# Kernel tuning notes

Measured on AMD Instinct MI355X. Metric: run time of the kernel, lower is better.

## Reference

```python
import jax, jax.numpy as jnp
import numpy as np

EPS = 1e-8  # matches torch F.cosine_similarity eps


def setup_inputs() -> dict:
    key = jax.random.key(0)
    k1, k2, k3 = jax.random.split(key, 3)
    S, B, H = 16, 512, 2048
    OGLogits = jax.random.normal(k1, (B, H), dtype=jnp.float32)
    enhancedSamplesLogits = jax.random.normal(k2, (S, B, H), dtype=jnp.float32)
    W = jax.random.normal(k3, (H, H), dtype=jnp.float32) * (1.0 / np.sqrt(H))
    b = jnp.zeros((H,), dtype=jnp.float32)
    return {"OGLogits": OGLogits, "enhancedSamplesLogits": enhancedSamplesLogits, "W": W, "b": b}


def reference(OGLogits, enhancedSamplesLogits, W, b):
    # Original torch code builds the full (S*B, B) cosine-similarity matrix and
    # keeps only the diagonal via an eye mask; mathematically that equals the
    # per-pair cosine similarity cos(enhanced[s,b], OG[b]), computed directly here.
    e_norm = jnp.linalg.norm(enhancedSamplesLogits, axis=-1)          # (S, B)
    o_norm = jnp.linalg.norm(OGLogits, axis=-1)                       # (B,)
    dots = jnp.einsum('sbh,bh->sb', enhancedSamplesLogits, OGLogits)  # (S, B)
    sims = dots / jnp.maximum(e_norm * o_norm[None, :], EPS)          # (S, B)
    weighted = enhancedSamplesLogits * sims[..., None]                # (S, B, H)
    weightedRep = weighted.mean(axis=0)                               # (B, H)
    return weightedRep @ W.T + b                                      # (B, H)
```

## Files before the change

kernel.cpp:

```cpp
#include <hip/hip_runtime.h>

#define S_DIM 16
#define B_DIM 512
#define H_DIM 2048
#define EPS 1e-8f

typedef short bf16x8 __attribute__((ext_vector_type(8)));
typedef float f32x4 __attribute__((ext_vector_type(4)));

__device__ __forceinline__ unsigned short f2bf(float f) {
    union { float f; unsigned int u; } v; v.f = f;
    unsigned int u = v.u;
    unsigned int r = (u + 0x7fffu + ((u >> 16) & 1u)) >> 16;
    return (unsigned short)r;
}

__device__ __forceinline__ float dot4(const float4& a, const float4& b) {
    return a.x*b.x + a.y*b.y + a.z*b.z + a.w*b.w;
}

__global__ __launch_bounds__(256) void convert_w_kernel(
    const float* __restrict__ W, unsigned short* __restrict__ Wb) {
    int i = blockIdx.x * 256 + threadIdx.x;
    float4 v = ((const float4*)W)[i];
    ushort4 o;
    o.x = f2bf(v.x); o.y = f2bf(v.y); o.z = f2bf(v.z); o.w = f2bf(v.w);
    ((ushort4*)Wb)[i] = o;
}

__global__ __launch_bounds__(512) void simwrep_kernel(
    const float* __restrict__ OG, const float* __restrict__ E,
    unsigned short* __restrict__ wrep) {
    const int b = blockIdx.x;
    const int t = threadIdx.x;
    const int lane = t & 63;
    const int wave = t >> 6;

    __shared__ float4 buf[8][512];

    const float4* og4 = (const float4*)(OG + (size_t)b * H_DIM);
    float4 og[8];
    float og2 = 0.f;
    #pragma unroll
    for (int i = 0; i < 8; ++i) {
        og[i] = og4[i * 64 + lane];
        og2 += dot4(og[i], og[i]);
    }
    #pragma unroll
    for (int m = 32; m >= 1; m >>= 1) og2 += __shfl_xor(og2, m, 64);
    const float onorm = sqrtf(og2);

    const int s0 = wave * 2, s1 = wave * 2 + 1;
    const float4* e40 = (const float4*)(E + ((size_t)s0 * B_DIM + b) * H_DIM);
    const float4* e41 = (const float4*)(E + ((size_t)s1 * B_DIM + b) * H_DIM);
    float4 e0[8], e1[8];
    float d0 = 0.f, d1 = 0.f, n0 = 0.f, n1 = 0.f;
    #pragma unroll
    for (int i = 0; i < 8; ++i) {
        e0[i] = e40[i * 64 + lane];
        e1[i] = e41[i * 64 + lane];
        d0 += dot4(e0[i], og[i]);
        n0 += dot4(e0[i], e0[i]);
        d1 += dot4(e1[i], og[i]);
        n1 += dot4(e1[i], e1[i]);
    }
    #pragma unroll
    for (int m = 32; m >= 1; m >>= 1) {
        d0 += __shfl_xor(d0, m, 64);
        n0 += __shfl_xor(n0, m, 64);
        d1 += __shfl_xor(d1, m, 64);
        n1 += __shfl_xor(n1, m, 64);
    }
    const float sim0 = d0 / fmaxf(sqrtf(n0) * onorm, EPS);
    const float sim1 = d1 / fmaxf(sqrtf(n1) * onorm, EPS);

    #pragma unroll
    for (int i = 0; i < 8; ++i) {
        float4 p;
        p.x = e0[i].x * sim0 + e1[i].x * sim1;
        p.y = e0[i].y * sim0 + e1[i].y * sim1;
        p.z = e0[i].z * sim0 + e1[i].z * sim1;
        p.w = e0[i].w * sim0 + e1[i].w * sim1;
        buf[wave][i * 64 + lane] = p;
    }
    __syncthreads();

    float4 s = buf[0][t];
    #pragma unroll
    for (int w = 1; w < 8; ++w) {
        float4 v = buf[w][t];
        s.x += v.x; s.y += v.y; s.z += v.z; s.w += v.w;
    }
    const float sc = 1.f / (float)S_DIM;
    ushort4 o;
    o.x = f2bf(s.x * sc); o.y = f2bf(s.y * sc);
    o.z = f2bf(s.z * sc); o.w = f2bf(s.w * sc);
    ((ushort4*)wrep)[(size_t)b * (H_DIM / 4) + t] = o;
}

__global__ __launch_bounds__(256) void gemm_kernel(
    const unsigned short* __restrict__ A, const unsigned short* __restrict__ Bw,
    const float* __restrict__ bias, float* __restrict__ out) {
    const int n0 = blockIdx.x * 64;
    const int m0 = blockIdx.y * 64;

    __shared__ unsigned short As[64][40];
    __shared__ unsigned short Bs[64][40];

    const int t = threadIdx.x;
    const int lane = t & 63;
    const int wave = t >> 6;
    const int wm = (wave & 1) * 32;
    const int wn = (wave >> 1) * 32;
    const int lr = t >> 2;
    const int lq = t & 3;

    const size_t aoff = (size_t)(m0 + lr) * H_DIM + lq * 8;
    const size_t boff = (size_t)(n0 + lr) * H_DIM + lq * 8;

    f32x4 acc00 = {0.f, 0.f, 0.f, 0.f};
    f32x4 acc01 = {0.f, 0.f, 0.f, 0.f};
    f32x4 acc10 = {0.f, 0.f, 0.f, 0.f};
    f32x4 acc11 = {0.f, 0.f, 0.f, 0.f};

    const int row = lane & 15;
    const int q = lane >> 4;

    uint4 av = *(const uint4*)(A + aoff);
    uint4 bv = *(const uint4*)(Bw + boff);

    for (int k0 = 0; k0 < H_DIM; k0 += 32) {
        *(uint4*)&As[lr][lq * 8] = av;
        *(uint4*)&Bs[lr][lq * 8] = bv;
        __syncthreads();
        if (k0 + 32 < H_DIM) {
            av = *(const uint4*)(A + aoff + k0 + 32);
            bv = *(const uint4*)(Bw + boff + k0 + 32);
        }
        bf16x8 a0 = *(const bf16x8*)&As[wm + row][q * 8];
        bf16x8 a1 = *(const bf16x8*)&As[wm + 16 + row][q * 8];
        bf16x8 b0 = *(const bf16x8*)&Bs[wn + row][q * 8];
        bf16x8 b1 = *(const bf16x8*)&Bs[wn + 16 + row][q * 8];
        acc00 = __builtin_amdgcn_mfma_f32_16x16x32_bf16(a0, b0, acc00, 0, 0, 0);
        acc01 = __builtin_amdgcn_mfma_f32_16x16x32_bf16(a0, b1, acc01, 0, 0, 0);
        acc10 = __builtin_amdgcn_mfma_f32_16x16x32_bf16(a1, b0, acc10, 0, 0, 0);
        acc11 = __builtin_amdgcn_mfma_f32_16x16x32_bf16(a1, b1, acc11, 0, 0, 0);
        __syncthreads();
    }

    const int col = lane & 15;
    const float bias0 = bias[n0 + wn + col];
    const float bias1 = bias[n0 + wn + 16 + col];
    #pragma unroll
    for (int r = 0; r < 4; ++r) {
        const int mr = q * 4 + r;
        float* o0 = out + (size_t)(m0 + wm + mr) * H_DIM + n0 + wn;
        float* o1 = out + (size_t)(m0 + wm + 16 + mr) * H_DIM + n0 + wn;
        o0[col]      = acc00[r] + bias0;
        o0[16 + col] = acc01[r] + bias1;
        o1[col]      = acc10[r] + bias0;
        o1[16 + col] = acc11[r] + bias1;
    }
}

extern "C" void kernel_launch(void* const* d_in, const int* in_sizes, int n_in,
                              void* d_out, int out_size, void* d_ws, size_t ws_size,
                              hipStream_t stream) {
    const float* OG   = (const float*)d_in[0];
    const float* E    = (const float*)d_in[1];
    const float* W    = (const float*)d_in[2];
    const float* bias = (const float*)d_in[3];
    float* out = (float*)d_out;

    unsigned short* wrep = (unsigned short*)d_ws;
    unsigned short* Wb   = wrep + (size_t)B_DIM * H_DIM;

    convert_w_kernel<<<(H_DIM * H_DIM / 4) / 256, 256, 0, stream>>>(W, Wb);
    simwrep_kernel<<<B_DIM, 512, 0, stream>>>(OG, E, wrep);
    gemm_kernel<<<dim3(H_DIM / 64, B_DIM / 64), 256, 0, stream>>>(wrep, Wb, bias, out);
}
```

Before: 131.9 us.

## Fuse W bf16 conversion into split-K GEMM and widen simwrep blocks

Removes the separate W fp32-to-bf16 conversion kernel and converts W tiles on the fly while they are loaded into the GEMM. The GEMM is split along K into two halves to double the block count, with a new reduce kernel that sums the partials and adds the bias. The similarity kernel now uses 1024 threads with one wave per sample instead of two samples per wave. In exchange, each W element is read as fp32 by multiple M-blocks and converted repeatedly, and the split-K path adds a fp32 partial buffer write and read.

```diff
diff --git a/kernel.cpp b/kernel.cpp
--- a/kernel.cpp
+++ b/kernel.cpp
@@ -19,16 +19,7 @@
     return a.x*b.x + a.y*b.y + a.z*b.z + a.w*b.w;
 }
 
-__global__ __launch_bounds__(256) void convert_w_kernel(
-    const float* __restrict__ W, unsigned short* __restrict__ Wb) {
-    int i = blockIdx.x * 256 + threadIdx.x;
-    float4 v = ((const float4*)W)[i];
-    ushort4 o;
-    o.x = f2bf(v.x); o.y = f2bf(v.y); o.z = f2bf(v.z); o.w = f2bf(v.w);
-    ((ushort4*)Wb)[i] = o;
-}
-
-__global__ __launch_bounds__(512) void simwrep_kernel(
+__global__ __launch_bounds__(1024) void simwrep_kernel(
     const float* __restrict__ OG, const float* __restrict__ E,
     unsigned short* __restrict__ wrep) {
     const int b = blockIdx.x;
@@ -36,7 +27,7 @@
     const int lane = t & 63;
     const int wave = t >> 6;
 
-    __shared__ float4 buf[8][512];
+    __shared__ float4 buf[16][512];
 
     const float4* og4 = (const float4*)(OG + (size_t)b * H_DIM);
     float4 og[8];
@@ -50,62 +41,56 @@
     for (int m = 32; m >= 1; m >>= 1) og2 += __shfl_xor(og2, m, 64);
     const float onorm = sqrtf(og2);
 
-    const int s0 = wave * 2, s1 = wave * 2 + 1;
-    const float4* e40 = (const float4*)(E + ((size_t)s0 * B_DIM + b) * H_DIM);
-    const float4* e41 = (const float4*)(E + ((size_t)s1 * B_DIM + b) * H_DIM);
-    float4 e0[8], e1[8];
-    float d0 = 0.f, d1 = 0.f, n0 = 0.f, n1 = 0.f;
+    const float4* e4 = (const float4*)(E + ((size_t)wave * B_DIM + b) * H_DIM);
+    float4 e[8];
+    float d = 0.f, n = 0.f;
     #pragma unroll
     for (int i = 0; i < 8; ++i) {
-        e0[i] = e40[i * 64 + lane];
-        e1[i] = e41[i * 64 + lane];
-        d0 += dot4(e0[i], og[i]);
-        n0 += dot4(e0[i], e0[i]);
-        d1 += dot4(e1[i], og[i]);
-        n1 += dot4(e1[i], e1[i]);
+        e[i] = e4[i * 64 + lane];
+        d += dot4(e[i], og[i]);
+        n += dot4(e[i], e[i]);
     }
     #pragma unroll
     for (int m = 32; m >= 1; m >>= 1) {
-        d0 += __shfl_xor(d0, m, 64);
-        n0 += __shfl_xor(n0, m, 64);
-        d1 += __shfl_xor(d1, m, 64);
-        n1 += __shfl_xor(n1, m, 64);
+        d += __shfl_xor(d, m, 64);
+        n += __shfl_xor(n, m, 64);
     }
-    const float sim0 = d0 / fmaxf(sqrtf(n0) * onorm, EPS);
-    const float sim1 = d1 / fmaxf(sqrtf(n1) * onorm, EPS);
+    const float sim = d / fmaxf(sqrtf(n) * onorm, EPS);
 
     #pragma unroll
     for (int i = 0; i < 8; ++i) {
         float4 p;
-        p.x = e0[i].x * sim0 + e1[i].x * sim1;
-        p.y = e0[i].y * sim0 + e1[i].y * sim1;
-        p.z = e0[i].z * sim0 + e1[i].z * sim1;
-        p.w = e0[i].w * sim0 + e1[i].w * sim1;
+        p.x = e[i].x * sim; p.y = e[i].y * sim;
+        p.z = e[i].z * sim; p.w = e[i].w * sim;
         buf[wave][i * 64 + lane] = p;
     }
     __syncthreads();
 
-    float4 s = buf[0][t];
-    #pragma unroll
-    for (int w = 1; w < 8; ++w) {
-        float4 v = buf[w][t];
-        s.x += v.x; s.y += v.y; s.z += v.z; s.w += v.w;
+    if (t < 512) {
+        float4 s = buf[0][t];
+        #pragma unroll
+        for (int w = 1; w < 16; ++w) {
+            float4 v = buf[w][t];
+            s.x += v.x; s.y += v.y; s.z += v.z; s.w += v.w;
+        }
+        const float sc = 1.f / (float)S_DIM;
+        ushort4 o;
+        o.x = f2bf(s.x * sc); o.y = f2bf(s.y * sc);
+        o.z = f2bf(s.z * sc); o.w = f2bf(s.w * sc);
+        ((ushort4*)wrep)[(size_t)b * (H_DIM / 4) + t] = o;
     }
-    const float sc = 1.f / (float)S_DIM;
-    ushort4 o;
-    o.x = f2bf(s.x * sc); o.y = f2bf(s.y * sc);
-    o.z = f2bf(s.z * sc); o.w = f2bf(s.w * sc);
-    ((ushort4*)wrep)[(size_t)b * (H_DIM / 4) + t] = o;
 }
 
-__global__ __launch_bounds__(256) void gemm_kernel(
-    const unsigned short* __restrict__ A, const unsigned short* __restrict__ Bw,
-    const float* __restrict__ bias, float* __restrict__ out) {
+__global__ __launch_bounds__(256) void gemm_splitk_kernel(
+    const unsigned short* __restrict__ A, const float* __restrict__ W,
+    float* __restrict__ partial) {
     const int n0 = blockIdx.x * 64;
     const int m0 = blockIdx.y * 64;
+    const int kz = blockIdx.z;
+    const int kbase = kz * (H_DIM / 2);
 
     __shared__ unsigned short As[64][40];
-    __shared__ unsigned short Bs[64][40];
+    __shared__ unsigned short Ws[64][40];
 
     const int t = threadIdx.x;
     const int lane = t & 63;
@@ -115,8 +100,8 @@
     const int lr = t >> 2;
     const int lq = t & 3;
 
-    const size_t aoff = (size_t)(m0 + lr) * H_DIM + lq * 8;
-    const size_t boff = (size_t)(n0 + lr) * H_DIM + lq * 8;
+    const size_t aoff = (size_t)(m0 + lr) * H_DIM + kbase + lq * 8;
+    const float* wp = W + (size_t)(n0 + lr) * H_DIM + kbase + lq * 8;
 
     f32x4 acc00 = {0.f, 0.f, 0.f, 0.f};
     f32x4 acc01 = {0.f, 0.f, 0.f, 0.f};
@@ -127,20 +112,26 @@
     const int q = lane >> 4;
 
     uint4 av = *(const uint4*)(A + aoff);
-    uint4 bv = *(const uint4*)(Bw + boff);
+    float4 wv0 = *(const float4*)(wp);
+    float4 wv1 = *(const float4*)(wp + 4);
 
-    for (int k0 = 0; k0 < H_DIM; k0 += 32) {
+    for (int k0 = 0; k0 < H_DIM / 2; k0 += 32) {
         *(uint4*)&As[lr][lq * 8] = av;
-        *(uint4*)&Bs[lr][lq * 8] = bv;
+        ushort4 wlo, whi;
+        wlo.x = f2bf(wv0.x); wlo.y = f2bf(wv0.y); wlo.z = f2bf(wv0.z); wlo.w = f2bf(wv0.w);
+        whi.x = f2bf(wv1.x); whi.y = f2bf(wv1.y); whi.z = f2bf(wv1.z); whi.w = f2bf(wv1.w);
+        *(ushort4*)&Ws[lr][lq * 8] = wlo;
+        *(ushort4*)&Ws[lr][lq * 8 + 4] = whi;
         __syncthreads();
-        if (k0 + 32 < H_DIM) {
+        if (k0 + 32 < H_DIM / 2) {
             av = *(const uint4*)(A + aoff + k0 + 32);
-            bv = *(const uint4*)(Bw + boff + k0 + 32);
+            wv0 = *(const float4*)(wp + k0 + 32);
+            wv1 = *(const float4*)(wp + k0 + 36);
         }
         bf16x8 a0 = *(const bf16x8*)&As[wm + row][q * 8];
         bf16x8 a1 = *(const bf16x8*)&As[wm + 16 + row][q * 8];
-        bf16x8 b0 = *(const bf16x8*)&Bs[wn + row][q * 8];
-        bf16x8 b1 = *(const bf16x8*)&Bs[wn + 16 + row][q * 8];
+        bf16x8 b0 = *(const bf16x8*)&Ws[wn + row][q * 8];
+        bf16x8 b1 = *(const bf16x8*)&Ws[wn + 16 + row][q * 8];
         acc00 = __builtin_amdgcn_mfma_f32_16x16x32_bf16(a0, b0, acc00, 0, 0, 0);
         acc01 = __builtin_amdgcn_mfma_f32_16x16x32_bf16(a0, b1, acc01, 0, 0, 0);
         acc10 = __builtin_amdgcn_mfma_f32_16x16x32_bf16(a1, b0, acc10, 0, 0, 0);
@@ -148,19 +139,31 @@
         __syncthreads();
     }
 
+    float* pz = partial + (size_t)kz * B_DIM * H_DIM;
     const int col = lane & 15;
-    const float bias0 = bias[n0 + wn + col];
-    const float bias1 = bias[n0 + wn + 16 + col];
     #pragma unroll
     for (int r = 0; r < 4; ++r) {
         const int mr = q * 4 + r;
-        float* o0 = out + (size_t)(m0 + wm + mr) * H_DIM + n0 + wn;
-        float* o1 = out + (size_t)(m0 + wm + 16 + mr) * H_DIM + n0 + wn;
-        o0[col]      = acc00[r] + bias0;
-        o0[16 + col] = acc01[r] + bias1;
-        o1[col]      = acc10[r] + bias0;
-        o1[16 + col] = acc11[r] + bias1;
+        float* o0 = pz + (size_t)(m0 + wm + mr) * H_DIM + n0 + wn;
+        float* o1 = pz + (size_t)(m0 + wm + 16 + mr) * H_DIM + n0 + wn;
+        o0[col]      = acc00[r];
+        o0[16 + col] = acc01[r];
+        o1[col]      = acc10[r];
+        o1[16 + col] = acc11[r];
     }
+}
+
+__global__ __launch_bounds__(256) void reduce_kernel(
+    const float* __restrict__ partial, const float* __restrict__ bias,
+    float* __restrict__ out) {
+    const int i = blockIdx.x * 256 + threadIdx.x;
+    const float4 a = ((const float4*)partial)[i];
+    const float4 c = ((const float4*)partial)[i + B_DIM * H_DIM / 4];
+    const float4 bs = ((const float4*)bias)[i & (H_DIM / 4 - 1)];
+    float4 o;
+    o.x = a.x + c.x + bs.x; o.y = a.y + c.y + bs.y;
+    o.z = a.z + c.z + bs.z; o.w = a.w + c.w + bs.w;
+    ((float4*)out)[i] = o;
 }
 
 extern "C" void kernel_launch(void* const* d_in, const int* in_sizes, int n_in,
@@ -173,9 +176,9 @@
     float* out = (float*)d_out;
 
     unsigned short* wrep = (unsigned short*)d_ws;
-    unsigned short* Wb   = wrep + (size_t)B_DIM * H_DIM;
+    float* partial = (float*)((char*)d_ws + (size_t)B_DIM * H_DIM * 2);
 
-    convert_w_kernel<<<(H_DIM * H_DIM / 4) / 256, 256, 0, stream>>>(W, Wb);
-    simwrep_kernel<<<B_DIM, 512, 0, stream>>>(OG, E, wrep);
-    gemm_kernel<<<dim3(H_DIM / 64, B_DIM / 64), 256, 0, stream>>>(wrep, Wb, bias, out);
+    simwrep_kernel<<<B_DIM, 1024, 0, stream>>>(OG, E, wrep);
+    gemm_splitk_kernel<<<dim3(H_DIM / 64, B_DIM / 64, 2), 256, 0, stream>>>(wrep, W, partial);
+    reduce_kernel<<<(B_DIM * H_DIM / 4) / 256, 256, 0, stream>>>(partial, bias, out);
 }
```

New measurement: 138.7 us. +5.2%, slower.

## Fuse W bf16 conversion into GEMM tile load and cut simwrep register pressure

Applied to the files above, without the earlier changes.

Removes the separate W-to-bf16 conversion kernel and instead loads fp32 W tiles directly in the GEMM, converting to bf16 in registers before the shared-memory store. This saves a 16MB read and 8MB write plus one launch. The cost is that each W element is now reread in fp32 by all 8 M-blocks (twice the bytes per reread) and converted redundantly. The K tile grows to 64 with padded shared arrays. The simwrep kernel keeps OG in shared memory and processes samples sequentially, which lowers register use and raises occupancy through launch_bounds(512,4).

```diff
diff --git a/kernel.cpp b/kernel.cpp
--- a/kernel.cpp
+++ b/kernel.cpp
@@ -19,16 +19,7 @@
     return a.x*b.x + a.y*b.y + a.z*b.z + a.w*b.w;
 }
 
-__global__ __launch_bounds__(256) void convert_w_kernel(
-    const float* __restrict__ W, unsigned short* __restrict__ Wb) {
-    int i = blockIdx.x * 256 + threadIdx.x;
-    float4 v = ((const float4*)W)[i];
-    ushort4 o;
-    o.x = f2bf(v.x); o.y = f2bf(v.y); o.z = f2bf(v.z); o.w = f2bf(v.w);
-    ((ushort4*)Wb)[i] = o;
-}
-
-__global__ __launch_bounds__(512) void simwrep_kernel(
+__global__ __launch_bounds__(512, 4) void simwrep_kernel(
     const float* __restrict__ OG, const float* __restrict__ E,
     unsigned short* __restrict__ wrep) {
     const int b = blockIdx.x;
@@ -36,53 +27,55 @@
     const int lane = t & 63;
     const int wave = t >> 6;
 
+    __shared__ float4 ogs[512];
     __shared__ float4 buf[8][512];
+    __shared__ float red[8];
 
     const float4* og4 = (const float4*)(OG + (size_t)b * H_DIM);
-    float4 og[8];
+    float4 o = og4[t];
+    ogs[t] = o;
+    float p = dot4(o, o);
+    #pragma unroll
+    for (int m = 32; m >= 1; m >>= 1) p += __shfl_xor(p, m, 64);
+    if (lane == 0) red[wave] = p;
+    __syncthreads();
     float og2 = 0.f;
     #pragma unroll
-    for (int i = 0; i < 8; ++i) {
-        og[i] = og4[i * 64 + lane];
-        og2 += dot4(og[i], og[i]);
-    }
-    #pragma unroll
-    for (int m = 32; m >= 1; m >>= 1) og2 += __shfl_xor(og2, m, 64);
+    for (int w = 0; w < 8; ++w) og2 += red[w];
     const float onorm = sqrtf(og2);
 
-    const int s0 = wave * 2, s1 = wave * 2 + 1;
-    const float4* e40 = (const float4*)(E + ((size_t)s0 * B_DIM + b) * H_DIM);
-    const float4* e41 = (const float4*)(E + ((size_t)s1 * B_DIM + b) * H_DIM);
-    float4 e0[8], e1[8];
-    float d0 = 0.f, d1 = 0.f, n0 = 0.f, n1 = 0.f;
+    float4 acc[8];
     #pragma unroll
-    for (int i = 0; i < 8; ++i) {
-        e0[i] = e40[i * 64 + lane];
-        e1[i] = e41[i * 64 + lane];
-        d0 += dot4(e0[i], og[i]);
-        n0 += dot4(e0[i], e0[i]);
-        d1 += dot4(e1[i], og[i]);
-        n1 += dot4(e1[i], e1[i]);
-    }
-    #pragma unroll
-    for (int m = 32; m >= 1; m >>= 1) {
-        d0 += __shfl_xor(d0, m, 64);
-        n0 += __shfl_xor(n0, m, 64);
-        d1 += __shfl_xor(d1, m, 64);
-        n1 += __shfl_xor(n1, m, 64);
-    }
-    const float sim0 = d0 / fmaxf(sqrtf(n0) * onorm, EPS);
-    const float sim1 = d1 / fmaxf(sqrtf(n1) * onorm, EPS);
+    for (int i = 0; i < 8; ++i) acc[i] = make_float4(0.f, 0.f, 0.f, 0.f);
 
     #pragma unroll
-    for (int i = 0; i < 8; ++i) {
-        float4 p;
-        p.x = e0[i].x * sim0 + e1[i].x * sim1;
-        p.y = e0[i].y * sim0 + e1[i].y * sim1;
-        p.z = e0[i].z * sim0 + e1[i].z * sim1;
-        p.w = e0[i].w * sim0 + e1[i].w * sim1;
-        buf[wave][i * 64 + lane] = p;
+    for (int si = 0; si < 2; ++si) {
+        const int s = wave + si * 8;
+        const float4* e4 = (const float4*)(E + ((size_t)s * B_DIM + b) * H_DIM);
+        float4 e[8];
+        float d = 0.f, n = 0.f;
+        #pragma unroll
+        for (int i = 0; i < 8; ++i) {
+            e[i] = e4[i * 64 + lane];
+            float4 og = ogs[i * 64 + lane];
+            d += dot4(e[i], og);
+            n += dot4(e[i], e[i]);
+        }
+        #pragma unroll
+        for (int m = 32; m >= 1; m >>= 1) {
+            d += __shfl_xor(d, m, 64);
+            n += __shfl_xor(n, m, 64);
+        }
+        const float sim = d / fmaxf(sqrtf(n) * onorm, EPS);
+        #pragma unroll
+        for (int i = 0; i < 8; ++i) {
+            acc[i].x += e[i].x * sim; acc[i].y += e[i].y * sim;
+            acc[i].z += e[i].z * sim; acc[i].w += e[i].w * sim;
+        }
     }
+
+    #pragma unroll
+    for (int i = 0; i < 8; ++i) buf[wave][i * 64 + lane] = acc[i];
     __syncthreads();
 
     float4 s = buf[0][t];
@@ -92,20 +85,20 @@
         s.x += v.x; s.y += v.y; s.z += v.z; s.w += v.w;
     }
     const float sc = 1.f / (float)S_DIM;
-    ushort4 o;
-    o.x = f2bf(s.x * sc); o.y = f2bf(s.y * sc);
-    o.z = f2bf(s.z * sc); o.w = f2bf(s.w * sc);
-    ((ushort4*)wrep)[(size_t)b * (H_DIM / 4) + t] = o;
+    ushort4 ob;
+    ob.x = f2bf(s.x * sc); ob.y = f2bf(s.y * sc);
+    ob.z = f2bf(s.z * sc); ob.w = f2bf(s.w * sc);
+    ((ushort4*)wrep)[(size_t)b * (H_DIM / 4) + t] = ob;
 }
 
 __global__ __launch_bounds__(256) void gemm_kernel(
-    const unsigned short* __restrict__ A, const unsigned short* __restrict__ Bw,
+    const unsigned short* __restrict__ A, const float* __restrict__ W,
     const float* __restrict__ bias, float* __restrict__ out) {
     const int n0 = blockIdx.x * 64;
     const int m0 = blockIdx.y * 64;
 
-    __shared__ unsigned short As[64][40];
-    __shared__ unsigned short Bs[64][40];
+    __shared__ unsigned short As[64][72];
+    __shared__ unsigned short Ws[64][72];
 
     const int t = threadIdx.x;
     const int lane = t & 63;
@@ -115,8 +108,8 @@
     const int lr = t >> 2;
     const int lq = t & 3;
 
-    const size_t aoff = (size_t)(m0 + lr) * H_DIM + lq * 8;
-    const size_t boff = (size_t)(n0 + lr) * H_DIM + lq * 8;
+    const unsigned short* ap = A + (size_t)(m0 + lr) * H_DIM + lq * 16;
+    const float* wp = W + (size_t)(n0 + lr) * H_DIM + lq * 16;
 
     f32x4 acc00 = {0.f, 0.f, 0.f, 0.f};
     f32x4 acc01 = {0.f, 0.f, 0.f, 0.f};
@@ -126,25 +119,45 @@
     const int row = lane & 15;
     const int q = lane >> 4;
 
-    uint4 av = *(const uint4*)(A + aoff);
-    uint4 bv = *(const uint4*)(Bw + boff);
+    uint4 av0 = *(const uint4*)(ap);
+    uint4 av1 = *(const uint4*)(ap + 8);
+    float4 wv0 = *(const float4*)(wp);
+    float4 wv1 = *(const float4*)(wp + 4);
+    float4 wv2 = *(const float4*)(wp + 8);
+    float4 wv3 = *(const float4*)(wp + 12);
 
-    for (int k0 = 0; k0 < H_DIM; k0 += 32) {
-        *(uint4*)&As[lr][lq * 8] = av;
-        *(uint4*)&Bs[lr][lq * 8] = bv;
+    for (int k0 = 0; k0 < H_DIM; k0 += 64) {
+        *(uint4*)&As[lr][lq * 16] = av0;
+        *(uint4*)&As[lr][lq * 16 + 8] = av1;
+        ushort4 c0, c1, c2, c3;
+        c0.x = f2bf(wv0.x); c0.y = f2bf(wv0.y); c0.z = f2bf(wv0.z); c0.w = f2bf(wv0.w);
+        c1.x = f2bf(wv1.x); c1.y = f2bf(wv1.y); c1.z = f2bf(wv1.z); c1.w = f2bf(wv1.w);
+        c2.x = f2bf(wv2.x); c2.y = f2bf(wv2.y); c2.z = f2bf(wv2.z); c2.w = f2bf(wv2.w);
+        c3.x = f2bf(wv3.x); c3.y = f2bf(wv3.y); c3.z = f2bf(wv3.z); c3.w = f2bf(wv3.w);
+        *(ushort4*)&Ws[lr][lq * 16]      = c0;
+        *(ushort4*)&Ws[lr][lq * 16 + 4]  = c1;
+        *(ushort4*)&Ws[lr][lq * 16 + 8]  = c2;
+        *(ushort4*)&Ws[lr][lq * 16 + 12] = c3;
         __syncthreads();
-        if (k0 + 32 < H_DIM) {
-            av = *(const uint4*)(A + aoff + k0 + 32);
-            bv = *(const uint4*)(Bw + boff + k0 + 32);
+        if (k0 + 64 < H_DIM) {
+            av0 = *(const uint4*)(ap + k0 + 64);
+            av1 = *(const uint4*)(ap + k0 + 72);
+            wv0 = *(const float4*)(wp + k0 + 64);
+            wv1 = *(const float4*)(wp + k0 + 68);
+            wv2 = *(const float4*)(wp + k0 + 72);
+            wv3 = *(const float4*)(wp + k0 + 76);
         }
-        bf16x8 a0 = *(const bf16x8*)&As[wm + row][q * 8];
-        bf16x8 a1 = *(const bf16x8*)&As[wm + 16 + row][q * 8];
-        bf16x8 b0 = *(const bf16x8*)&Bs[wn + row][q * 8];
-        bf16x8 b1 = *(const bf16x8*)&Bs[wn + 16 + row][q * 8];
-        acc00 = __builtin_amdgcn_mfma_f32_16x16x32_bf16(a0, b0, acc00, 0, 0, 0);
-        acc01 = __builtin_amdgcn_mfma_f32_16x16x32_bf16(a0, b1, acc01, 0, 0, 0);
-        acc10 = __builtin_amdgcn_mfma_f32_16x16x32_bf16(a1, b0, acc10, 0, 0, 0);
-        acc11 = __builtin_amdgcn_mfma_f32_16x16x32_bf16(a1, b1, acc11, 0, 0, 0);
+        #pragma unroll
+        for (int ks = 0; ks < 2; ++ks) {
+            bf16x8 a0 = *(const bf16x8*)&As[wm + row][ks * 32 + q * 8];
+            bf16x8 a1 = *(const bf16x8*)&As[wm + 16 + row][ks * 32 + q * 8];
+            bf16x8 b0 = *(const bf16x8*)&Ws[wn + row][ks * 32 + q * 8];
+            bf16x8 b1 = *(const bf16x8*)&Ws[wn + 16 + row][ks * 32 + q * 8];
+            acc00 = __builtin_amdgcn_mfma_f32_16x16x32_bf16(a0, b0, acc00, 0, 0, 0);
+            acc01 = __builtin_amdgcn_mfma_f32_16x16x32_bf16(a0, b1, acc01, 0, 0, 0);
+            acc10 = __builtin_amdgcn_mfma_f32_16x16x32_bf16(a1, b0, acc10, 0, 0, 0);
+            acc11 = __builtin_amdgcn_mfma_f32_16x16x32_bf16(a1, b1, acc11, 0, 0, 0);
+        }
         __syncthreads();
     }
 
@@ -173,9 +186,7 @@
     float* out = (float*)d_out;
 
     unsigned short* wrep = (unsigned short*)d_ws;
-    unsigned short* Wb   = wrep + (size_t)B_DIM * H_DIM;
 
-    convert_w_kernel<<<(H_DIM * H_DIM / 4) / 256, 256, 0, stream>>>(W, Wb);
     simwrep_kernel<<<B_DIM, 512, 0, stream>>>(OG, E, wrep);
-    gemm_kernel<<<dim3(H_DIM / 64, B_DIM / 64), 256, 0, stream>>>(wrep, Wb, bias, out);
+    gemm_kernel<<<dim3(H_DIM / 64, B_DIM / 64), 256, 0, stream>>>(wrep, W, bias, out);
 }
```

Result: slower. 139.0 us (+5.4%).
